# Performance work log

Measured on AMD Instinct MI355X. Metric: run time of the kernel, lower is better.

The kernel has to match this reference:

```python
import jax, jax.numpy as jnp
import numpy as np

B, T, C, H, R = 2, 2048, 2048, 16, 8
D = C // H  # head_dim = 128


def _rope_cache(seq_len, dim, theta=10000.0):
    pos = jnp.arange(seq_len, dtype=jnp.float32)[:, None]            # [T,1]
    idx = jnp.arange(0, dim, 2, dtype=jnp.float32)                   # [D/2]
    freqs = 1.0 / (theta ** (idx / dim))
    ang = pos * freqs                                                # [T, D/2]
    return jnp.cos(ang), jnp.sin(ang)


def setup_inputs() -> dict:
    key = jax.random.key(0)
    ks = jax.random.split(key, 16)
    s = 0.02
    inp = {"x": jax.random.normal(ks[0], (B, T, C), dtype=jnp.float32)}
    i = 1
    for nm in ("q", "k", "v", "p"):
        inp[f"{nm}_w"] = jax.random.normal(ks[i], (C, C), dtype=jnp.float32) * s; i += 1
        inp[f"{nm}_b"] = jnp.zeros((C,), dtype=jnp.float32)
        inp[f"{nm}_A"] = jax.random.normal(ks[i], (C, R), dtype=jnp.float32) * s; i += 1
        inp[f"{nm}_B"] = jax.random.normal(ks[i], (R, C), dtype=jnp.float32) * s; i += 1
    cos, sin = _rope_cache(T, D)
    inp["cos"] = cos
    inp["sin"] = sin
    inp["mask"] = jnp.tril(jnp.ones((T, T), dtype=bool))  # causal SDPA mask
    inp["use_lora"] = 1
    return inp


def _lora_linear(x, w, b, A, Bm, use_lora):
    # base GEMM + bias, plus low-rank adapter x @ A @ B (intended path)
    out = x @ w.T + b
    if use_lora:
        out = out + (x @ A) @ Bm
    return out


def _apply_rope(x, cos, sin):
    # x: [B,H,T,D]; cos/sin: [T, D/2] broadcast over batch & heads
    x1 = x[..., ::2]
    x2 = x[..., 1::2]
    y = jnp.stack((x1 * cos - x2 * sin, x1 * sin + x2 * cos), axis=-1)
    return y.reshape(x.shape)


def reference(x, q_w, q_b, q_A, q_B, k_w, k_b, k_A, k_B,
              v_w, v_b, v_A, v_B, p_w, p_b, p_A, p_B,
              cos, sin, mask, use_lora):
    Bsz, Tl, Cd = x.shape
    q = _lora_linear(x, q_w, q_b, q_A, q_B, use_lora).reshape(Bsz, Tl, H, D).transpose(0, 2, 1, 3)
    k = _lora_linear(x, k_w, k_b, k_A, k_B, use_lora).reshape(Bsz, Tl, H, D).transpose(0, 2, 1, 3)
    v = _lora_linear(x, v_w, v_b, v_A, v_B, use_lora).reshape(Bsz, Tl, H, D).transpose(0, 2, 1, 3)
    q = _apply_rope(q, cos, sin)
    k = _apply_rope(k, cos, sin)
    # scaled dot-product attention with boolean mask (True = attend)
    scale = 1.0 / jnp.sqrt(jnp.asarray(D, dtype=x.dtype))
    scores = jnp.einsum('bhqd,bhkd->bhqk', q, k) * scale          # [B,H,T,T]
    neg = jnp.asarray(jnp.finfo(scores.dtype).min, dtype=scores.dtype)
    scores = jnp.where(mask, scores, neg)
    attn = jax.nn.softmax(scores, axis=-1)
    out = jnp.einsum('bhqk,bhkd->bhqd', attn, v)                  # [B,H,T,D]
    y = out.transpose(0, 2, 1, 3).reshape(Bsz, Tl, Cd)
    return _lora_linear(y, p_w, p_b, p_A, p_B, use_lora)
```

## Files before the change

kernel.cpp:

```cpp
#include <hip/hip_runtime.h>

typedef _Float16 f16;
typedef _Float16 f16x4 __attribute__((ext_vector_type(4)));
typedef _Float16 f16x8 __attribute__((ext_vector_type(8)));
typedef __fp16 hf2 __attribute__((ext_vector_type(2)));
typedef float f32x4 __attribute__((ext_vector_type(4)));

#define DEV static __device__ __forceinline__

DEV void gl_lds16(const void* g, void* l) {
  __builtin_amdgcn_global_load_lds(
      (const __attribute__((address_space(1))) void*)g,
      (__attribute__((address_space(3))) void*)l, 16, 0, 0);
}

DEV uint pkrtz(float a, float b) {
  hf2 h = __builtin_amdgcn_cvt_pkrtz(a, b);
  return __builtin_bit_cast(uint, h);
}

__global__ void cast_f16_kernel(const float* __restrict__ x,
                                const float* __restrict__ w0,
                                const float* __restrict__ w1,
                                const float* __restrict__ w2,
                                const float* __restrict__ w3,
                                f16* __restrict__ xb, f16* __restrict__ b0,
                                f16* __restrict__ b1, f16* __restrict__ b2,
                                f16* __restrict__ b3) {
  const int total4 = (8388608 + 4 * 4194304) / 4;
  for (int i = blockIdx.x * blockDim.x + threadIdx.x; i < total4;
       i += gridDim.x * blockDim.x) {
    int e = i << 2;
    const float* s; f16* d; int off;
    if (e < 8388608)        { s = x;  d = xb; off = e; }
    else if (e < 12582912)  { s = w0; d = b0; off = e - 8388608; }
    else if (e < 16777216)  { s = w1; d = b1; off = e - 12582912; }
    else if (e < 20971520)  { s = w2; d = b2; off = e - 16777216; }
    else                    { s = w3; d = b3; off = e - 20971520; }
    float4 v = *(const float4*)(s + off);
    f16x4 hv = {(f16)v.x, (f16)v.y, (f16)v.z, (f16)v.w};
    *(f16x4*)(d + off) = hv;
  }
}

__global__ __launch_bounds__(256) void lora_x_kernel(
    const float* __restrict__ x, const float* __restrict__ Aq,
    const float* __restrict__ Ak, const float* __restrict__ Av,
    float* __restrict__ la) {
  const int wave = threadIdx.x >> 6, lane = threadIdx.x & 63;
  const int m = blockIdx.x * 4 + wave;
  const float* xrow = x + (size_t)m * 2048;
  const float* As[3] = {Aq, Ak, Av};
  float acc[3][8] = {};
  for (int i = 0; i < 32; ++i) {
    int k = i * 64 + lane;
    float xv = xrow[k];
#pragma unroll
    for (int nm = 0; nm < 3; ++nm) {
      const float4* ap = (const float4*)(As[nm] + (size_t)k * 8);
      float4 a0 = ap[0], a1 = ap[1];
      acc[nm][0] += xv * a0.x; acc[nm][1] += xv * a0.y;
      acc[nm][2] += xv * a0.z; acc[nm][3] += xv * a0.w;
      acc[nm][4] += xv * a1.x; acc[nm][5] += xv * a1.y;
      acc[nm][6] += xv * a1.z; acc[nm][7] += xv * a1.w;
    }
  }
#pragma unroll
  for (int nm = 0; nm < 3; ++nm)
#pragma unroll
    for (int r = 0; r < 8; ++r) {
      float v = acc[nm][r];
#pragma unroll
      for (int off = 1; off < 64; off <<= 1) v += __shfl_xor(v, off);
      acc[nm][r] = v;
    }
  if (lane == 0) {
#pragma unroll
    for (int nm = 0; nm < 3; ++nm)
#pragma unroll
      for (int r = 0; r < 8; ++r)
        la[nm * 32768 + (size_t)m * 8 + r] = acc[nm][r];
  }
}

__global__ __launch_bounds__(256) void lora_p_kernel(
    const f16* __restrict__ y, const float* __restrict__ Ap,
    float* __restrict__ lap) {
  const int wave = threadIdx.x >> 6, lane = threadIdx.x & 63;
  const int m = blockIdx.x * 4 + wave;
  const f16* yrow = y + (size_t)m * 2048;
  float acc[8] = {};
  for (int i = 0; i < 4; ++i) {
    int k0 = i * 512 + lane * 8;
    f16x8 yv = *(const f16x8*)(yrow + k0);
#pragma unroll
    for (int j = 0; j < 8; ++j) {
      float xv = (float)yv[j];
      const float4* ap = (const float4*)(Ap + (size_t)(k0 + j) * 8);
      float4 a0 = ap[0], a1 = ap[1];
      acc[0] += xv * a0.x; acc[1] += xv * a0.y;
      acc[2] += xv * a0.z; acc[3] += xv * a0.w;
      acc[4] += xv * a1.x; acc[5] += xv * a1.y;
      acc[6] += xv * a1.z; acc[7] += xv * a1.w;
    }
  }
#pragma unroll
  for (int r = 0; r < 8; ++r) {
    float v = acc[r];
#pragma unroll
    for (int off = 1; off < 64; off <<= 1) v += __shfl_xor(v, off);
    acc[r] = v;
  }
  if (lane == 0) {
#pragma unroll
    for (int r = 0; r < 8; ++r) lap[(size_t)m * 8 + r] = acc[r];
  }
}

template <int MODE>
__global__ __launch_bounds__(256, 2) void gemm_kernel(
    const f16* __restrict__ A, const f16* __restrict__ Bw,
    const float* __restrict__ bias, const float* __restrict__ la,
    const float* __restrict__ Bm, const int* __restrict__ use_lora,
    const float* __restrict__ cosT, const float* __restrict__ sinT,
    void* __restrict__ out) {
  __shared__ char smem[32768];
  const int tid = threadIdx.x;
  const int wave = tid >> 6, lane = tid & 63;
  const int lr = lane & 15, lg = lane >> 4;
  const int bm = blockIdx.x >> 4, bn = blockIdx.x & 15;
  const int m0 = bm << 7, n0 = bn << 7;
  const int wr = wave >> 1, wc = wave & 1;

  uint aoff[4], boff[4];
#pragma unroll
  for (int r = 0; r < 4; ++r) {
    uint beta = (uint)(wave * 4 + r) * 1024 + (uint)lane * 16;
    uint row = beta >> 7;
    uint c = (beta & 127u) ^ ((row & 7u) << 4);
    aoff[r] = (uint)(m0 + row) * 4096 + c;
    boff[r] = (uint)(n0 + row) * 4096 + c;
  }
  const char* Ab = (const char*)A;
  const char* Bb = (const char*)Bw;

  f32x4 acc[4][4] = {};

  for (int kt = 0; kt < 32; ++kt) {
    __syncthreads();
    const int kb = kt << 7;
#pragma unroll
    for (int r = 0; r < 4; ++r) {
      gl_lds16(Ab + (size_t)(aoff[r] + kb), smem + (wave * 4 + r) * 1024);
      gl_lds16(Bb + (size_t)(boff[r] + kb), smem + 16384 + (wave * 4 + r) * 1024);
    }
    __syncthreads();

    f16x8 af[2][4], bf[2][4];
#pragma unroll
    for (int ks = 0; ks < 2; ++ks) {
#pragma unroll
      for (int mi = 0; mi < 4; ++mi) {
        int row = wr * 64 + mi * 16 + lr;
        int c = (ks * 64 + lg * 16) ^ ((row & 7) << 4);
        af[ks][mi] = *(const f16x8*)(smem + row * 128 + c);
      }
#pragma unroll
      for (int ni = 0; ni < 4; ++ni) {
        int row = wc * 64 + ni * 16 + lr;
        int c = (ks * 64 + lg * 16) ^ ((row & 7) << 4);
        bf[ks][ni] = *(const f16x8*)(smem + 16384 + row * 128 + c);
      }
    }
    __builtin_amdgcn_s_setprio(1);
#pragma unroll
    for (int ks = 0; ks < 2; ++ks)
#pragma unroll
      for (int mi = 0; mi < 4; ++mi)
#pragma unroll
        for (int ni = 0; ni < 4; ++ni)
          acc[mi][ni] = __builtin_amdgcn_mfma_f32_16x16x32_f16(
              af[ks][mi], bf[ks][ni], acc[mi][ni], 0, 0, 0);
    __builtin_amdgcn_s_setprio(0);
  }

  const int ul = use_lora[0];
  __syncthreads();

  float bv[4], bml[4][8];
#pragma unroll
  for (int ni = 0; ni < 4; ++ni) {
    int n = n0 + wc * 64 + ni * 16 + lr;
    bv[ni] = bias[n];
    if (ul) {
#pragma unroll
      for (int r = 0; r < 8; ++r) bml[ni][r] = Bm[r * 2048 + n];
    }
  }

  f16* stg = (f16*)smem;
#pragma unroll
  for (int mi = 0; mi < 4; ++mi) {
    const int mbase = m0 + wr * 64 + mi * 16 + lg * 4;
    float lar[4][8];
    if (ul) {
#pragma unroll
      for (int rg = 0; rg < 4; ++rg) {
        const float4* lp = (const float4*)(la + (size_t)(mbase + rg) * 8);
        float4 l0 = lp[0], l1 = lp[1];
        lar[rg][0] = l0.x; lar[rg][1] = l0.y; lar[rg][2] = l0.z; lar[rg][3] = l0.w;
        lar[rg][4] = l1.x; lar[rg][5] = l1.y; lar[rg][6] = l1.z; lar[rg][7] = l1.w;
      }
    }
#pragma unroll
    for (int ni = 0; ni < 4; ++ni) {
      const int n = n0 + wc * 64 + ni * 16 + lr;
#pragma unroll
      for (int rg = 0; rg < 4; ++rg) {
        float v = acc[mi][ni][rg] + bv[ni];
        if (ul) {
#pragma unroll
          for (int r = 0; r < 8; ++r) v += lar[rg][r] * bml[ni][r];
        }
        if (MODE == 0) {
          float pv = __shfl_xor(v, 1);
          const int m = mbase + rg;
          const int t = m & 2047;
          const int d = n & 127;
          const int ci = t * 64 + (d >> 1);
          float cs = cosT[ci], sn = sinT[ci];
          float res = ((lane & 1) == 0) ? (v * cs - pv * sn)
                                        : (pv * sn + v * cs);
          stg[(wr * 64 + mi * 16 + lg * 4 + rg) * 128 +
              (wc * 64 + ni * 16 + lr)] = (f16)res;
        } else if (MODE == 1) {
          stg[(wr * 64 + mi * 16 + lg * 4 + rg) * 128 +
              (wc * 64 + ni * 16 + lr)] = (f16)v;
        } else {
          ((float*)out)[(size_t)(mbase + rg) * 2048 + n] = v;
        }
      }
    }
  }

  if (MODE < 2) {
    __syncthreads();
    if (MODE == 0) {
      const long b_ = m0 >> 11;
      const int tb = m0 & 2047;
      char* obase = (char*)out + ((b_ * 16 + bn) * 2048 + tb) * 256;
#pragma unroll
      for (int p = 0; p < 8; ++p) {
        int s = p * 4096 + tid * 16;
        int row = s >> 8, c = s & 255;
        *(uint4*)(obase + (long)row * 256 + c) = *(const uint4*)(smem + s);
      }
    } else {
      char* obase = (char*)out + ((long)m0 * 2048 + n0) * 2;
#pragma unroll
      for (int p = 0; p < 8; ++p) {
        int s = p * 4096 + tid * 16;
        int row = s >> 8, c = s & 255;
        *(uint4*)(obase + (long)row * 4096 + c) = *(const uint4*)(smem + s);
      }
    }
  }
}

__global__ void transpose_v_kernel(const ushort* __restrict__ vbi,
                                   ushort* __restrict__ vto) {
  __shared__ ushort tile[32][33];
  const int t0 = blockIdx.x << 5;
  const int d0 = blockIdx.y << 5;
  const int bh = blockIdx.z;
  const int b = bh >> 4, h = bh & 15;
  const int tx = threadIdx.x, ty = threadIdx.y;
  const ushort* src = vbi + ((size_t)(b * 2048 + t0)) * 2048 + h * 128 + d0;
#pragma unroll
  for (int i = 0; i < 4; ++i)
    tile[ty + 8 * i][tx] = src[(size_t)(ty + 8 * i) * 2048 + tx];
  __syncthreads();
  ushort* dst = vto + ((size_t)bh * 128 + d0) * 2048 + t0;
#pragma unroll
  for (int i = 0; i < 4; ++i)
    dst[(size_t)(ty + 8 * i) * 2048 + tx] = tile[tx][ty + 8 * i];
}

__global__ __launch_bounds__(256, 2) void attn_kernel(
    const f16* __restrict__ qr, const f16* __restrict__ kr,
    const f16* __restrict__ vt, f16* __restrict__ y) {
  extern __shared__ char smem[];
  const int tid = threadIdx.x, wave = tid >> 6, lane = tid & 63;
  const int lr = lane & 15, lg = lane >> 4;
  const int qt = 15 - (int)blockIdx.x;
  const int q0 = qt << 7;
  const int h = blockIdx.y, b = blockIdx.z;
  const long bh = b * 16 + h;
  const int nt = 2 * qt + 2;

  const char* kbase = (const char*)kr + bh * 2048 * 256;
  const char* vbase = (const char*)vt + bh * 128 * 4096;

  f16x8 qf[2][4];
#pragma unroll
  for (int g = 0; g < 2; ++g) {
    const char* qb =
        (const char*)qr + (bh * 2048 + q0 + wave * 32 + g * 16 + lr) * 256;
#pragma unroll
    for (int ks = 0; ks < 4; ++ks)
      qf[g][ks] = *(const f16x8*)(qb + ks * 64 + lg * 16);
  }

  f32x4 o[2][8] = {};
  float mrow[2] = {-3e38f, -3e38f};
  float lsum[2] = {0.f, 0.f};
  const float SC2 = 0.12752551286084103f;

  auto STAGE = [&](int kv0, int bsel) {
    char* Ks = smem + bsel * 32768;
    char* Vs = Ks + 16384;
#pragma unroll
    for (int r = 0; r < 4; ++r) {
      uint s = (uint)(wave * 4 + r) * 1024 + (uint)lane * 16;
      uint rowk = s >> 8, ck = (s & 255u) ^ ((rowk & 7u) << 4);
      gl_lds16(kbase + (size_t)(kv0 + rowk) * 256 + ck,
               Ks + (wave * 4 + r) * 1024);
      uint rowv = s >> 7, cv = (s & 127u) ^ ((rowv & 7u) << 4);
      gl_lds16(vbase + (size_t)rowv * 4096 + kv0 * 2 + cv,
               Vs + (wave * 4 + r) * 1024);
    }
  };

  STAGE(0, 0);
  __syncthreads();

  for (int kt = 0; kt < nt; ++kt) {
    const int kv0 = kt << 6;
    if (kt + 1 < nt) STAGE((kt + 1) << 6, (kt + 1) & 1);
    const char* Ks = smem + (kt & 1) * 32768;
    const char* Vs = Ks + 16384;

    if (kv0 <= q0 + wave * 32 + 31) {
      f32x4 sa[2][4] = {};
      __builtin_amdgcn_s_setprio(1);
#pragma unroll
      for (int ks = 0; ks < 4; ++ks)
#pragma unroll
        for (int n = 0; n < 4; ++n) {
          int row = n * 16 + lr;
          int c = (ks * 64 + lg * 16) ^ ((row & 7) << 4);
          f16x8 kf = *(const f16x8*)(Ks + row * 256 + c);
          sa[0][n] =
              __builtin_amdgcn_mfma_f32_16x16x32_f16(kf, qf[0][ks], sa[0][n], 0, 0, 0);
          sa[1][n] =
              __builtin_amdgcn_mfma_f32_16x16x32_f16(kf, qf[1][ks], sa[1][n], 0, 0, 0);
        }
      __builtin_amdgcn_s_setprio(0);

      f16x8 pf[2][2];
#pragma unroll
      for (int g = 0; g < 2; ++g) {
        const int qgbase = q0 + wave * 32 + g * 16;
        float L[16];
        float pm = -3e38f;
        const bool dm = (kv0 + 63 > qgbase);
#pragma unroll
        for (int n = 0; n < 4; ++n)
#pragma unroll
          for (int rg = 0; rg < 4; ++rg) {
            float Lv = sa[g][n][rg] * SC2;
            if (dm && (kv0 + n * 16 + lg * 4 + rg > qgbase + lr)) Lv = -3e37f;
            L[n * 4 + rg] = Lv;
            pm = fmaxf(pm, Lv);
          }
        pm = fmaxf(pm, __shfl_xor(pm, 16));
        pm = fmaxf(pm, __shfl_xor(pm, 32));
        float mn = fmaxf(mrow[g], pm);
        float alpha = exp2f(mrow[g] - mn);
        mrow[g] = mn;
        float ps = 0.f;
#pragma unroll
        for (int i = 0; i < 16; ++i) {
          float p = exp2f(L[i] - mn);
          L[i] = p;
          ps += p;
        }
        ps += __shfl_xor(ps, 16);
        ps += __shfl_xor(ps, 32);
        lsum[g] = lsum[g] * alpha + ps;
#pragma unroll
        for (int dt = 0; dt < 8; ++dt)
#pragma unroll
          for (int rg = 0; rg < 4; ++rg) o[g][dt][rg] *= alpha;

#pragma unroll
        for (int ks2 = 0; ks2 < 2; ++ks2) {
          uint w0 = pkrtz(L[8 * ks2 + 0], L[8 * ks2 + 1]);
          uint w1 = pkrtz(L[8 * ks2 + 2], L[8 * ks2 + 3]);
          uint w2 = pkrtz(L[8 * ks2 + 4], L[8 * ks2 + 5]);
          uint w3 = pkrtz(L[8 * ks2 + 6], L[8 * ks2 + 7]);
          int src1 = ((lg & 1) << 5) + lr;
          int src2 = src1 + 16;
          uint a0 = __shfl((int)w0, src1), a1 = __shfl((int)w1, src1);
          uint a2 = __shfl((int)w2, src1), a3 = __shfl((int)w3, src1);
          uint b0 = __shfl((int)w0, src2), b1 = __shfl((int)w1, src2);
          uint b2 = __shfl((int)w2, src2), b3 = __shfl((int)w3, src2);
          const bool hi = (lg >> 1) != 0;
          uint4 uu;
          uu.x = hi ? a2 : a0;
          uu.y = hi ? a3 : a1;
          uu.z = hi ? b2 : b0;
          uu.w = hi ? b3 : b1;
          pf[g][ks2] = __builtin_bit_cast(f16x8, uu);
        }
      }

#pragma unroll
      for (int ks2 = 0; ks2 < 2; ++ks2) {
        __builtin_amdgcn_s_setprio(1);
#pragma unroll
        for (int dt = 0; dt < 8; ++dt) {
          int drow = dt * 16 + lr;
          int c = (ks2 * 64 + lg * 16) ^ ((drow & 7) << 4);
          f16x8 vf = *(const f16x8*)(Vs + drow * 128 + c);
          o[0][dt] =
              __builtin_amdgcn_mfma_f32_16x16x32_f16(vf, pf[0][ks2], o[0][dt], 0, 0, 0);
          o[1][dt] =
              __builtin_amdgcn_mfma_f32_16x16x32_f16(vf, pf[1][ks2], o[1][dt], 0, 0, 0);
        }
        __builtin_amdgcn_s_setprio(0);
      }
    }
    __syncthreads();
  }

#pragma unroll
  for (int g = 0; g < 2; ++g) {
    const float inv = 1.f / lsum[g];
    const int row = wave * 32 + g * 16 + lr;
#pragma unroll
    for (int dt = 0; dt < 8; ++dt) {
      uint lo = pkrtz(o[g][dt][0] * inv, o[g][dt][1] * inv);
      uint hi2 = pkrtz(o[g][dt][2] * inv, o[g][dt][3] * inv);
      int c = (dt * 32 + lg * 8) ^ ((row & 7) << 4);
      uint2 w;
      w.x = lo;
      w.y = hi2;
      *(uint2*)(smem + row * 256 + c) = w;
    }
  }
  __syncthreads();
#pragma unroll
  for (int p = 0; p < 8; ++p) {
    int s = p * 4096 + tid * 16;
    int row = s >> 8, cb = s & 255;
    int c = cb ^ ((row & 7) << 4);
    char* dst =
        (char*)y + ((long)(b * 2048 + q0 + row) * 2048 + h * 128) * 2 + cb;
    *(uint4*)dst = *(const uint4*)(smem + row * 256 + c);
  }
}

extern "C" void kernel_launch(void* const* d_in, const int* in_sizes, int n_in,
                              void* d_out, int out_size, void* d_ws,
                              size_t ws_size, hipStream_t stream) {
  (void)in_sizes; (void)n_in; (void)out_size; (void)ws_size;
  const float* x   = (const float*)d_in[0];
  const float* q_w = (const float*)d_in[1];
  const float* q_b = (const float*)d_in[2];
  const float* q_A = (const float*)d_in[3];
  const float* q_B = (const float*)d_in[4];
  const float* k_w = (const float*)d_in[5];
  const float* k_b = (const float*)d_in[6];
  const float* k_A = (const float*)d_in[7];
  const float* k_B = (const float*)d_in[8];
  const float* v_w = (const float*)d_in[9];
  const float* v_b = (const float*)d_in[10];
  const float* v_A = (const float*)d_in[11];
  const float* v_B = (const float*)d_in[12];
  const float* p_w = (const float*)d_in[13];
  const float* p_b = (const float*)d_in[14];
  const float* p_A = (const float*)d_in[15];
  const float* p_B = (const float*)d_in[16];
  const float* cosT = (const float*)d_in[17];
  const float* sinT = (const float*)d_in[18];
  const int* use_lora = (const int*)d_in[20];

  char* ws = (char*)d_ws;
  f16* xb  = (f16*)(ws);
  f16* wqb = (f16*)(ws + 16777216);
  f16* wkb = (f16*)(ws + 25165824);
  f16* wvb = (f16*)(ws + 33554432);
  f16* wpb = (f16*)(ws + 41943040);
  float* la = (float*)(ws + 50331648);
  f16* qr  = (f16*)(ws + 50855936);
  f16* kr  = (f16*)(ws + 67633152);
  f16* vb  = (f16*)(ws + 84410368);
  f16* vt  = (f16*)(ws);
  f16* y   = vb;
  float* lap = la + 98304;

  cast_f16_kernel<<<dim3(2048), dim3(256), 0, stream>>>(
      x, q_w, k_w, v_w, p_w, xb, wqb, wkb, wvb, wpb);
  lora_x_kernel<<<dim3(1024), dim3(256), 0, stream>>>(x, q_A, k_A, v_A, la);
  gemm_kernel<0><<<dim3(512), dim3(256), 0, stream>>>(
      xb, wqb, q_b, la, q_B, use_lora, cosT, sinT, (void*)qr);
  gemm_kernel<0><<<dim3(512), dim3(256), 0, stream>>>(
      xb, wkb, k_b, la + 32768, k_B, use_lora, cosT, sinT, (void*)kr);
  gemm_kernel<1><<<dim3(512), dim3(256), 0, stream>>>(
      xb, wvb, v_b, la + 65536, v_B, use_lora, nullptr, nullptr, (void*)vb);
  transpose_v_kernel<<<dim3(64, 4, 32), dim3(32, 8), 0, stream>>>(
      (const ushort*)vb, (ushort*)vt);
  attn_kernel<<<dim3(16, 16, 2), dim3(256), 65536, stream>>>(qr, kr, vt, y);
  lora_p_kernel<<<dim3(1024), dim3(256), 0, stream>>>(y, p_A, lap);
  gemm_kernel<2><<<dim3(512), dim3(256), 0, stream>>>(
      y, wpb, p_b, lap, p_B, use_lora, nullptr, nullptr, d_out);
}
```

Measured before the change: 393.4 us.

## Triple-buffer GEMM with 512-thread 128x256 tiles and lazy softmax rescale

Reworks the projection GEMM to use 512-thread blocks computing 128x256 tiles. A three-stage LDS ring, sized through dynamic shared memory, issues global-to-LDS loads two k-steps ahead, and the MFMA quarters are interleaved with partial loads and barriers. This is meant to hide the load latency of the old single-buffered loop, which synchronised twice per k-step. The attention kernel also skips the online-softmax rescale of the accumulator unless the running max grows by more than a threshold. That saves multiplies but risks fp16 overflow margins on the P values. The epilogue staging is swizzled and widened to the new tile shape.

```diff
diff --git a/kernel.cpp b/kernel.cpp
--- a/kernel.cpp
+++ b/kernel.cpp
@@ -17,6 +17,10 @@
 DEV uint pkrtz(float a, float b) {
   hf2 h = __builtin_amdgcn_cvt_pkrtz(a, b);
   return __builtin_bit_cast(uint, h);
+}
+
+DEV f32x4 MFMA(f16x8 a, f16x8 b, f32x4 c) {
+  return __builtin_amdgcn_mfma_f32_16x16x32_f16(a, b, c, 0, 0, 0);
 }
 
 __global__ void cast_f16_kernel(const float* __restrict__ x,
@@ -118,75 +122,115 @@
 }
 
 template <int MODE>
-__global__ __launch_bounds__(256, 2) void gemm_kernel(
+__global__ __launch_bounds__(512, 1) void gemm_kernel(
     const f16* __restrict__ A, const f16* __restrict__ Bw,
     const float* __restrict__ bias, const float* __restrict__ la,
     const float* __restrict__ Bm, const int* __restrict__ use_lora,
     const float* __restrict__ cosT, const float* __restrict__ sinT,
     void* __restrict__ out) {
-  __shared__ char smem[32768];
+  extern __shared__ char smem[];
   const int tid = threadIdx.x;
   const int wave = tid >> 6, lane = tid & 63;
   const int lr = lane & 15, lg = lane >> 4;
-  const int bm = blockIdx.x >> 4, bn = blockIdx.x & 15;
-  const int m0 = bm << 7, n0 = bn << 7;
-  const int wr = wave >> 1, wc = wave & 1;
-
-  uint aoff[4], boff[4];
-#pragma unroll
-  for (int r = 0; r < 4; ++r) {
-    uint beta = (uint)(wave * 4 + r) * 1024 + (uint)lane * 16;
-    uint row = beta >> 7;
-    uint c = (beta & 127u) ^ ((row & 7u) << 4);
-    aoff[r] = (uint)(m0 + row) * 4096 + c;
-    boff[r] = (uint)(n0 + row) * 4096 + c;
-  }
+  const int bm = (int)blockIdx.x >> 3, bn = (int)blockIdx.x & 7;
+  const int m0 = bm << 7, n0 = bn << 8;
+  const int wr = wave >> 2, wc = wave & 3;
+
   const char* Ab = (const char*)A;
   const char* Bb = (const char*)Bw;
 
+  auto stageA = [&](int kt, int bsel, int sw) {
+    uint base = (uint)sw * 8192u + (uint)wave * 1024u;
+    uint idx = base + (uint)lane * 16u;
+    uint row = idx >> 7, cb = idx & 127u;
+    uint c = cb ^ ((row & 7u) << 4);
+    gl_lds16(Ab + (size_t)(m0 + row) * 4096 + (size_t)kt * 128 + c,
+             smem + bsel * 49152 + base);
+  };
+  auto stageB = [&](int kt, int bsel, int sw) {
+    uint base = (uint)sw * 8192u + (uint)wave * 1024u;
+    uint idx = base + (uint)lane * 16u;
+    uint row = idx >> 7, cb = idx & 127u;
+    uint c = cb ^ ((row & 7u) << 4);
+    gl_lds16(Bb + (size_t)(n0 + row) * 4096 + (size_t)kt * 128 + c,
+             smem + bsel * 49152 + 16384 + base);
+  };
+  auto rdA = [&](int bsel, int ks, int mi) -> f16x8 {
+    int row = wr * 64 + mi * 16 + lr;
+    int c = (ks * 64 + lg * 16) ^ ((row & 7) << 4);
+    return *(const f16x8*)(smem + bsel * 49152 + row * 128 + c);
+  };
+  auto rdB = [&](int bsel, int ks, int ni) -> f16x8 {
+    int row = wc * 64 + ni * 16 + lr;
+    int c = (ks * 64 + lg * 16) ^ ((row & 7) << 4);
+    return *(const f16x8*)(smem + bsel * 49152 + 16384 + row * 128 + c);
+  };
+
   f32x4 acc[4][4] = {};
 
+#pragma unroll
+  for (int sw = 0; sw < 2; ++sw) stageA(0, 0, sw);
+#pragma unroll
+  for (int sw = 0; sw < 4; ++sw) stageB(0, 0, sw);
+#pragma unroll
+  for (int sw = 0; sw < 2; ++sw) stageA(1, 1, sw);
+#pragma unroll
+  for (int sw = 0; sw < 4; ++sw) stageB(1, 1, sw);
+
   for (int kt = 0; kt < 32; ++kt) {
-    __syncthreads();
-    const int kb = kt << 7;
-#pragma unroll
-    for (int r = 0; r < 4; ++r) {
-      gl_lds16(Ab + (size_t)(aoff[r] + kb), smem + (wave * 4 + r) * 1024);
-      gl_lds16(Bb + (size_t)(boff[r] + kb), smem + 16384 + (wave * 4 + r) * 1024);
-    }
-    __syncthreads();
-
-    f16x8 af[2][4], bf[2][4];
-#pragma unroll
-    for (int ks = 0; ks < 2; ++ks) {
-#pragma unroll
-      for (int mi = 0; mi < 4; ++mi) {
-        int row = wr * 64 + mi * 16 + lr;
-        int c = (ks * 64 + lg * 16) ^ ((row & 7) << 4);
-        af[ks][mi] = *(const f16x8*)(smem + row * 128 + c);
-      }
-#pragma unroll
-      for (int ni = 0; ni < 4; ++ni) {
-        int row = wc * 64 + ni * 16 + lr;
-        int c = (ks * 64 + lg * 16) ^ ((row & 7) << 4);
-        bf[ks][ni] = *(const f16x8*)(smem + 16384 + row * 128 + c);
-      }
-    }
+    const int cur = kt % 3;
+    const int nxt = (kt + 2) % 3;
+    const bool st = (kt + 2 < 32);
+    if (kt == 31) asm volatile("s_waitcnt vmcnt(0)" ::: "memory");
+    else         asm volatile("s_waitcnt vmcnt(6)" ::: "memory");
+    __builtin_amdgcn_s_barrier();
+
+    f16x8 a0, a1, a2, a3, b0, b1;
+    a0 = rdA(cur, 0, 0); a1 = rdA(cur, 0, 1);
+    a2 = rdA(cur, 0, 2); a3 = rdA(cur, 0, 3);
+    b0 = rdB(cur, 0, 0); b1 = rdB(cur, 0, 1);
+    if (st) { stageA(kt + 2, nxt, 0); stageA(kt + 2, nxt, 1); }
     __builtin_amdgcn_s_setprio(1);
-#pragma unroll
-    for (int ks = 0; ks < 2; ++ks)
-#pragma unroll
-      for (int mi = 0; mi < 4; ++mi)
-#pragma unroll
-        for (int ni = 0; ni < 4; ++ni)
-          acc[mi][ni] = __builtin_amdgcn_mfma_f32_16x16x32_f16(
-              af[ks][mi], bf[ks][ni], acc[mi][ni], 0, 0, 0);
+    acc[0][0] = MFMA(a0, b0, acc[0][0]); acc[1][0] = MFMA(a1, b0, acc[1][0]);
+    acc[2][0] = MFMA(a2, b0, acc[2][0]); acc[3][0] = MFMA(a3, b0, acc[3][0]);
+    acc[0][1] = MFMA(a0, b1, acc[0][1]); acc[1][1] = MFMA(a1, b1, acc[1][1]);
+    acc[2][1] = MFMA(a2, b1, acc[2][1]); acc[3][1] = MFMA(a3, b1, acc[3][1]);
     __builtin_amdgcn_s_setprio(0);
-  }
+    __builtin_amdgcn_s_barrier();
+
+    b0 = rdB(cur, 0, 2); b1 = rdB(cur, 0, 3);
+    if (st) { stageB(kt + 2, nxt, 0); stageB(kt + 2, nxt, 1); }
+    __builtin_amdgcn_s_setprio(1);
+    acc[0][2] = MFMA(a0, b0, acc[0][2]); acc[1][2] = MFMA(a1, b0, acc[1][2]);
+    acc[2][2] = MFMA(a2, b0, acc[2][2]); acc[3][2] = MFMA(a3, b0, acc[3][2]);
+    acc[0][3] = MFMA(a0, b1, acc[0][3]); acc[1][3] = MFMA(a1, b1, acc[1][3]);
+    acc[2][3] = MFMA(a2, b1, acc[2][3]); acc[3][3] = MFMA(a3, b1, acc[3][3]);
+    __builtin_amdgcn_s_setprio(0);
+    __builtin_amdgcn_s_barrier();
+
+    a0 = rdA(cur, 1, 0); a1 = rdA(cur, 1, 1);
+    a2 = rdA(cur, 1, 2); a3 = rdA(cur, 1, 3);
+    b0 = rdB(cur, 1, 0); b1 = rdB(cur, 1, 1);
+    if (st) { stageB(kt + 2, nxt, 2); stageB(kt + 2, nxt, 3); }
+    __builtin_amdgcn_s_setprio(1);
+    acc[0][0] = MFMA(a0, b0, acc[0][0]); acc[1][0] = MFMA(a1, b0, acc[1][0]);
+    acc[2][0] = MFMA(a2, b0, acc[2][0]); acc[3][0] = MFMA(a3, b0, acc[3][0]);
+    acc[0][1] = MFMA(a0, b1, acc[0][1]); acc[1][1] = MFMA(a1, b1, acc[1][1]);
+    acc[2][1] = MFMA(a2, b1, acc[2][1]); acc[3][1] = MFMA(a3, b1, acc[3][1]);
+    __builtin_amdgcn_s_setprio(0);
+    __builtin_amdgcn_s_barrier();
+
+    b0 = rdB(cur, 1, 2); b1 = rdB(cur, 1, 3);
+    __builtin_amdgcn_s_setprio(1);
+    acc[0][2] = MFMA(a0, b0, acc[0][2]); acc[1][2] = MFMA(a1, b0, acc[1][2]);
+    acc[2][2] = MFMA(a2, b0, acc[2][2]); acc[3][2] = MFMA(a3, b0, acc[3][2]);
+    acc[0][3] = MFMA(a0, b1, acc[0][3]); acc[1][3] = MFMA(a1, b1, acc[1][3]);
+    acc[2][3] = MFMA(a2, b1, acc[2][3]); acc[3][3] = MFMA(a3, b1, acc[3][3]);
+    __builtin_amdgcn_s_setprio(0);
+  }
+  __builtin_amdgcn_s_barrier();
 
   const int ul = use_lora[0];
-  __syncthreads();
-
   float bv[4], bml[4][8];
 #pragma unroll
   for (int ni = 0; ni < 4; ++ni) {
@@ -198,7 +242,6 @@
     }
   }
 
-  f16* stg = (f16*)smem;
 #pragma unroll
   for (int mi = 0; mi < 4; ++mi) {
     const int mbase = m0 + wr * 64 + mi * 16 + lg * 4;
@@ -222,20 +265,20 @@
 #pragma unroll
           for (int r = 0; r < 8; ++r) v += lar[rg][r] * bml[ni][r];
         }
+        const int lrow = wr * 64 + mi * 16 + lg * 4 + rg;
         if (MODE == 0) {
           float pv = __shfl_xor(v, 1);
-          const int m = mbase + rg;
-          const int t = m & 2047;
+          const int t = (mbase + rg) & 2047;
           const int d = n & 127;
           const int ci = t * 64 + (d >> 1);
           float cs = cosT[ci], sn = sinT[ci];
           float res = ((lane & 1) == 0) ? (v * cs - pv * sn)
                                         : (pv * sn + v * cs);
-          stg[(wr * 64 + mi * 16 + lg * 4 + rg) * 128 +
-              (wc * 64 + ni * 16 + lr)] = (f16)res;
+          int cbyte = ((wc * 64 + ni * 16 + lr) * 2) ^ ((lrow & 7) << 4);
+          *(f16*)(smem + lrow * 512 + cbyte) = (f16)res;
         } else if (MODE == 1) {
-          stg[(wr * 64 + mi * 16 + lg * 4 + rg) * 128 +
-              (wc * 64 + ni * 16 + lr)] = (f16)v;
+          int cbyte = ((wc * 64 + ni * 16 + lr) * 2) ^ ((lrow & 7) << 4);
+          *(f16*)(smem + lrow * 512 + cbyte) = (f16)v;
         } else {
           ((float*)out)[(size_t)(mbase + rg) * 2048 + n] = v;
         }
@@ -244,24 +287,22 @@
   }
 
   if (MODE < 2) {
-    __syncthreads();
-    if (MODE == 0) {
-      const long b_ = m0 >> 11;
-      const int tb = m0 & 2047;
-      char* obase = (char*)out + ((b_ * 16 + bn) * 2048 + tb) * 256;
-#pragma unroll
-      for (int p = 0; p < 8; ++p) {
-        int s = p * 4096 + tid * 16;
-        int row = s >> 8, c = s & 255;
-        *(uint4*)(obase + (long)row * 256 + c) = *(const uint4*)(smem + s);
-      }
-    } else {
-      char* obase = (char*)out + ((long)m0 * 2048 + n0) * 2;
-#pragma unroll
-      for (int p = 0; p < 8; ++p) {
-        int s = p * 4096 + tid * 16;
-        int row = s >> 8, c = s & 255;
-        *(uint4*)(obase + (long)row * 4096 + c) = *(const uint4*)(smem + s);
+    __builtin_amdgcn_s_barrier();
+#pragma unroll
+    for (int p = 0; p < 8; ++p) {
+      int s = p * 8192 + tid * 16;
+      int row = s >> 9, cb = s & 511;
+      int c = cb ^ ((row & 7) << 4);
+      uint4 val = *(const uint4*)(smem + row * 512 + c);
+      if (MODE == 0) {
+        const long b_ = (m0 + row) >> 11;
+        const int tb = (m0 + row) & 2047;
+        const int head = 2 * bn + (cb >> 8);
+        char* dst = (char*)out + ((b_ * 16 + head) * 2048 + tb) * 256 + (cb & 255);
+        *(uint4*)dst = val;
+      } else {
+        char* dst = (char*)out + ((long)(m0 + row) * 2048 + bn * 256) * 2 + cb;
+        *(uint4*)dst = val;
       }
     }
   }
@@ -350,10 +391,8 @@
           int row = n * 16 + lr;
           int c = (ks * 64 + lg * 16) ^ ((row & 7) << 4);
           f16x8 kf = *(const f16x8*)(Ks + row * 256 + c);
-          sa[0][n] =
-              __builtin_amdgcn_mfma_f32_16x16x32_f16(kf, qf[0][ks], sa[0][n], 0, 0, 0);
-          sa[1][n] =
-              __builtin_amdgcn_mfma_f32_16x16x32_f16(kf, qf[1][ks], sa[1][n], 0, 0, 0);
+          sa[0][n] = MFMA(kf, qf[0][ks], sa[0][n]);
+          sa[1][n] = MFMA(kf, qf[1][ks], sa[1][n]);
         }
       __builtin_amdgcn_s_setprio(0);
 
@@ -375,9 +414,17 @@
           }
         pm = fmaxf(pm, __shfl_xor(pm, 16));
         pm = fmaxf(pm, __shfl_xor(pm, 32));
-        float mn = fmaxf(mrow[g], pm);
-        float alpha = exp2f(mrow[g] - mn);
-        mrow[g] = mn;
+        if (!__all(pm - mrow[g] <= 8.f)) {
+          float mn = fmaxf(mrow[g], pm);
+          float alpha = exp2f(mrow[g] - mn);
+          mrow[g] = mn;
+          lsum[g] *= alpha;
+#pragma unroll
+          for (int dt = 0; dt < 8; ++dt)
+#pragma unroll
+            for (int rg = 0; rg < 4; ++rg) o[g][dt][rg] *= alpha;
+        }
+        const float mn = mrow[g];
         float ps = 0.f;
 #pragma unroll
         for (int i = 0; i < 16; ++i) {
@@ -387,11 +434,7 @@
         }
         ps += __shfl_xor(ps, 16);
         ps += __shfl_xor(ps, 32);
-        lsum[g] = lsum[g] * alpha + ps;
-#pragma unroll
-        for (int dt = 0; dt < 8; ++dt)
-#pragma unroll
-          for (int rg = 0; rg < 4; ++rg) o[g][dt][rg] *= alpha;
+        lsum[g] += ps;
 
 #pragma unroll
         for (int ks2 = 0; ks2 < 2; ++ks2) {
@@ -423,10 +466,8 @@
           int drow = dt * 16 + lr;
           int c = (ks2 * 64 + lg * 16) ^ ((drow & 7) << 4);
           f16x8 vf = *(const f16x8*)(Vs + drow * 128 + c);
-          o[0][dt] =
-              __builtin_amdgcn_mfma_f32_16x16x32_f16(vf, pf[0][ks2], o[0][dt], 0, 0, 0);
-          o[1][dt] =
-              __builtin_amdgcn_mfma_f32_16x16x32_f16(vf, pf[1][ks2], o[1][dt], 0, 0, 0);
+          o[0][dt] = MFMA(vf, pf[0][ks2], o[0][dt]);
+          o[1][dt] = MFMA(vf, pf[1][ks2], o[1][dt]);
         }
         __builtin_amdgcn_s_setprio(0);
       }
@@ -503,16 +544,16 @@
   cast_f16_kernel<<<dim3(2048), dim3(256), 0, stream>>>(
       x, q_w, k_w, v_w, p_w, xb, wqb, wkb, wvb, wpb);
   lora_x_kernel<<<dim3(1024), dim3(256), 0, stream>>>(x, q_A, k_A, v_A, la);
-  gemm_kernel<0><<<dim3(512), dim3(256), 0, stream>>>(
+  gemm_kernel<0><<<dim3(256), dim3(512), 147456, stream>>>(
       xb, wqb, q_b, la, q_B, use_lora, cosT, sinT, (void*)qr);
-  gemm_kernel<0><<<dim3(512), dim3(256), 0, stream>>>(
+  gemm_kernel<0><<<dim3(256), dim3(512), 147456, stream>>>(
       xb, wkb, k_b, la + 32768, k_B, use_lora, cosT, sinT, (void*)kr);
-  gemm_kernel<1><<<dim3(512), dim3(256), 0, stream>>>(
+  gemm_kernel<1><<<dim3(256), dim3(512), 147456, stream>>>(
       xb, wvb, v_b, la + 65536, v_B, use_lora, nullptr, nullptr, (void*)vb);
   transpose_v_kernel<<<dim3(64, 4, 32), dim3(32, 8), 0, stream>>>(
       (const ushort*)vb, (ushort*)vt);
   attn_kernel<<<dim3(16, 16, 2), dim3(256), 65536, stream>>>(qr, kr, vt, y);
   lora_p_kernel<<<dim3(1024), dim3(256), 0, stream>>>(y, p_A, lap);
-  gemm_kernel<2><<<dim3(512), dim3(256), 0, stream>>>(
+  gemm_kernel<2><<<dim3(256), dim3(512), 147456, stream>>>(
       y, wpb, p_b, lap, p_B, use_lora, nullptr, nullptr, d_out);
 }
```

Measured after the change: 384.1 us. 1.02x faster.
